# Kernel tuning notes

Hardware: AMD Instinct MI355X
Metric: run time of the kernel (lower is better)

Reference implementation:

```python
import jax, jax.numpy as jnp
import numpy as np

B, D, L = 4, 64, 4096  # batch, pos feature dim (=pos_learnable_dim), sequence length

def setup_inputs() -> dict:
    key = jax.random.key(0)
    k1, k2 = jax.random.split(key, 2)
    pos_embed = jax.random.normal(k1, (B, D, L), dtype=jnp.float32)
    # _LinearWithBias(D, D): torch weight [out, in], bias [out]
    W_pos = (jax.random.normal(k2, (D, D), dtype=jnp.float32) / np.float32(np.sqrt(D)))
    b_pos = jnp.zeros((D,), dtype=jnp.float32)
    SOFTPLUS0 = 0.6931472  # softplus(0) = ln 2, gpytorch default raw param -> constrained value
    lengthscale = jnp.asarray(SOFTPLUS0, dtype=jnp.float32)   # RBFKernel lengthscale
    outputscale = jnp.asarray(SOFTPLUS0, dtype=jnp.float32)   # ScaleKernel outputscale
    return {"pos_embed": pos_embed, "W_pos": W_pos, "b_pos": b_pos,
            "lengthscale": lengthscale, "outputscale": outputscale}

def reference(pos_embed, W_pos, b_pos, lengthscale, outputscale):
    # pos_embed: [B, D, L]
    x = jnp.swapaxes(pos_embed, 1, 2)          # [B, L, D] (transpose, linear, transpose back, transpose again)
    x = x @ W_pos.T + b_pos                    # learnable positional linear on feature dim
    # gpytorch ScaleKernel(RBFKernel): outputscale * exp(-0.5 * ||(x_i - x_j)/lengthscale||^2)
    xs = x / lengthscale                       # [B, L, D]
    sq = jnp.sum(xs * xs, axis=-1)             # [B, L]
    sq_dist = sq[:, :, None] + sq[:, None, :] - 2.0 * jnp.einsum('bld,bmd->blm', xs, xs)
    sq_dist = jnp.maximum(sq_dist, 0.0)        # gpytorch clamps sq dist at 0
    return outputscale * jnp.exp(-0.5 * sq_dist)  # [B, L, L]
```

## Files before the change

kernel.cpp:

```cpp
#include <hip/hip_runtime.h>

using bf16x8 = __attribute__((ext_vector_type(8))) __bf16;
using f32x16 = __attribute__((ext_vector_type(16))) float;

#define BB 4
#define DD 64
#define LL 4096

__global__ __launch_bounds__(256) void prep_kernel(
    const float* __restrict__ pe,
    const float* __restrict__ W,
    const float* __restrict__ bias,
    const float* __restrict__ ls,
    __bf16* __restrict__ xs,
    float* __restrict__ h)
{
    __shared__ float pe_lds[DD][64];
    __shared__ float W_lds[DD * DD];
    __shared__ float hpart[4][64];

    const int tid = threadIdx.x;
    const int blk = blockIdx.x;
    const int b  = blk >> 6;
    const int l0 = (blk & 63) * 64;

    {
        const int l = tid & 63;
        const int kb = tid >> 6;
        #pragma unroll
        for (int it = 0; it < 16; ++it) {
            const int k = it * 4 + kb;
            pe_lds[k][l] = pe[((size_t)b * DD + k) * LL + l0 + l];
        }
    }
    #pragma unroll
    for (int it = 0; it < 16; ++it)
        W_lds[it * 256 + tid] = W[it * 256 + tid];
    __syncthreads();

    const int w = tid >> 6;
    const int l = tid & 63;
    const float SQRT_LOG2E = 1.2011224087864498f;
    const float scale = SQRT_LOG2E / ls[0];

    float acc[16];
    #pragma unroll
    for (int i = 0; i < 16; ++i) acc[i] = bias[w * 16 + i];

    for (int k4 = 0; k4 < 16; ++k4) {
        const float p0 = pe_lds[k4 * 4 + 0][l];
        const float p1 = pe_lds[k4 * 4 + 1][l];
        const float p2 = pe_lds[k4 * 4 + 2][l];
        const float p3 = pe_lds[k4 * 4 + 3][l];
        #pragma unroll
        for (int i = 0; i < 16; ++i) {
            const float4 wv = *(const float4*)&W_lds[(w * 16 + i) * DD + k4 * 4];
            acc[i] += p0 * wv.x + p1 * wv.y + p2 * wv.z + p3 * wv.w;
        }
    }

    unsigned short out16[16];
    float hs = 0.0f;
    #pragma unroll
    for (int i = 0; i < 16; ++i) {
        const float xf = acc[i] * scale;
        const __bf16 bv = (__bf16)xf;
        const float xr = (float)bv;
        hs += xr * xr;
        out16[i] = __builtin_bit_cast(unsigned short, bv);
    }
    {
        __bf16* dst = xs + ((size_t)b * LL + l0 + l) * DD + w * 16;
        *(uint4*)dst       = *(const uint4*)&out16[0];
        *(uint4*)(dst + 8) = *(const uint4*)&out16[8];
    }
    hpart[w][l] = hs;
    __syncthreads();
    if (tid < 64) {
        const float s = hpart[0][tid] + hpart[1][tid] + hpart[2][tid] + hpart[3][tid];
        h[(size_t)b * LL + tid + l0] = 0.5f * s;
    }
}

__global__ __launch_bounds__(256, 4) void gram_kernel(
    const __bf16* __restrict__ xs,
    const float* __restrict__ h,
    const float* __restrict__ osc,
    float* __restrict__ out)
{
    const int bid = blockIdx.x;
    const int b  = bid >> 10;
    const int t  = bid & 1023;
    const int ti = t >> 5, tj = t & 31;

    const int tid  = threadIdx.x;
    const int wid  = tid >> 6;
    const int lane = tid & 63;
    const int lr = lane & 31, lg = lane >> 5;

    const int rows0 = ti * 128 + (wid >> 1) * 64;
    const int cols0 = tj * 128 + (wid & 1) * 64;

    const __bf16* xsb = xs + (size_t)b * LL * DD;
    const float*  hb  = h + (size_t)b * LL;

    const float c  = osc[0];
    const float lc = __builtin_log2f(c);

    #pragma unroll 1
    for (int mt = 0; mt < 2; ++mt) {
        const int r0 = rows0 + mt * 32;

        bf16x8 af[4];
        #pragma unroll
        for (int kk = 0; kk < 4; ++kk)
            af[kk] = *(const bf16x8*)(xsb + (size_t)(r0 + lr) * DD + kk * 16 + lg * 8);

        float hi2[16];
        #pragma unroll
        for (int r = 0; r < 16; ++r)
            hi2[r] = hb[r0 + (r & 3) + 8 * (r >> 2) + 4 * lg] - lc;

        #pragma unroll 1
        for (int nt = 0; nt < 2; ++nt) {
            const int c0 = cols0 + nt * 32;

            bf16x8 bg[4];
            #pragma unroll
            for (int kk = 0; kk < 4; ++kk)
                bg[kk] = *(const bf16x8*)(xsb + (size_t)(c0 + lr) * DD + kk * 16 + lg * 8);

            f32x16 acc = (f32x16)(0.0f);
            #pragma unroll
            for (int kk = 0; kk < 4; ++kk)
                acc = __builtin_amdgcn_mfma_f32_32x32x16_bf16(af[kk], bg[kk], acc, 0, 0, 0);

            const int col = c0 + lr;
            const float hj = hb[col];
            float* op = out + ((size_t)b * LL + r0 + 4 * lg) * LL + col;
            #pragma unroll
            for (int r = 0; r < 16; ++r) {
                float tt = acc[r] - hi2[r] - hj;
                tt = fminf(tt, lc);
                const int rowoff = (r & 3) + 8 * (r >> 2);
                op[(size_t)rowoff * LL] = __builtin_amdgcn_exp2f(tt);
            }
        }
    }
}

extern "C" void kernel_launch(void* const* d_in, const int* in_sizes, int n_in,
                              void* d_out, int out_size, void* d_ws, size_t ws_size,
                              hipStream_t stream) {
    const float* pe   = (const float*)d_in[0];
    const float* W    = (const float*)d_in[1];
    const float* bias = (const float*)d_in[2];
    const float* ls   = (const float*)d_in[3];
    const float* osc  = (const float*)d_in[4];
    float* out = (float*)d_out;

    __bf16* xs = (__bf16*)d_ws;
    float*  h  = (float*)((char*)d_ws + (size_t)BB * LL * DD * 2);

    prep_kernel<<<256, 256, 0, stream>>>(pe, W, bias, ls, xs, h);
    gram_kernel<<<BB * 32 * 32, 256, 0, stream>>>(xs, h, osc, out);
}
```

Before: 75.03 us.

## Retile gram kernel to 32x512 block strips with full unrolling

```diff
diff --git a/kernel.cpp b/kernel.cpp
--- a/kernel.cpp
+++ b/kernel.cpp
@@ -82,7 +82,7 @@
     }
 }
 
-__global__ __launch_bounds__(256, 4) void gram_kernel(
+__global__ __launch_bounds__(256) void gram_kernel(
     const __bf16* __restrict__ xs,
     const float* __restrict__ h,
     const float* __restrict__ osc,
@@ -91,15 +91,16 @@
     const int bid = blockIdx.x;
     const int b  = bid >> 10;
     const int t  = bid & 1023;
-    const int ti = t >> 5, tj = t & 31;
+    const int ti = t >> 3;
+    const int tj = t & 7;
 
     const int tid  = threadIdx.x;
     const int wid  = tid >> 6;
     const int lane = tid & 63;
     const int lr = lane & 31, lg = lane >> 5;
 
-    const int rows0 = ti * 128 + (wid >> 1) * 64;
-    const int cols0 = tj * 128 + (wid & 1) * 64;
+    const int rows0 = ti * 32;
+    const int cols0 = tj * 512 + wid * 128;
 
     const __bf16* xsb = xs + (size_t)b * LL * DD;
     const float*  hb  = h + (size_t)b * LL;
@@ -107,44 +108,42 @@
     const float c  = osc[0];
     const float lc = __builtin_log2f(c);
 
-    #pragma unroll 1
-    for (int mt = 0; mt < 2; ++mt) {
-        const int r0 = rows0 + mt * 32;
-
-        bf16x8 af[4];
+    bf16x8 af[4], bg[4][4];
+    #pragma unroll
+    for (int kk = 0; kk < 4; ++kk)
+        af[kk] = *(const bf16x8*)(xsb + (size_t)(rows0 + lr) * DD + kk * 16 + lg * 8);
+    #pragma unroll
+    for (int nt = 0; nt < 4; ++nt)
         #pragma unroll
         for (int kk = 0; kk < 4; ++kk)
-            af[kk] = *(const bf16x8*)(xsb + (size_t)(r0 + lr) * DD + kk * 16 + lg * 8);
+            bg[nt][kk] = *(const bf16x8*)(xsb + (size_t)(cols0 + nt * 32 + lr) * DD + kk * 16 + lg * 8);
 
-        float hi2[16];
+    f32x16 acc[4];
+    #pragma unroll
+    for (int nt = 0; nt < 4; ++nt) acc[nt] = (f32x16)(0.0f);
+
+    #pragma unroll
+    for (int kk = 0; kk < 4; ++kk)
         #pragma unroll
-        for (int r = 0; r < 16; ++r)
-            hi2[r] = hb[r0 + (r & 3) + 8 * (r >> 2) + 4 * lg] - lc;
+        for (int nt = 0; nt < 4; ++nt)
+            acc[nt] = __builtin_amdgcn_mfma_f32_32x32x16_bf16(af[kk], bg[nt][kk], acc[nt], 0, 0, 0);
 
-        #pragma unroll 1
-        for (int nt = 0; nt < 2; ++nt) {
-            const int c0 = cols0 + nt * 32;
+    float hi2[16];
+    #pragma unroll
+    for (int r = 0; r < 16; ++r)
+        hi2[r] = hb[rows0 + (r & 3) + 8 * (r >> 2) + 4 * lg] - lc;
 
-            bf16x8 bg[4];
-            #pragma unroll
-            for (int kk = 0; kk < 4; ++kk)
-                bg[kk] = *(const bf16x8*)(xsb + (size_t)(c0 + lr) * DD + kk * 16 + lg * 8);
-
-            f32x16 acc = (f32x16)(0.0f);
-            #pragma unroll
-            for (int kk = 0; kk < 4; ++kk)
-                acc = __builtin_amdgcn_mfma_f32_32x32x16_bf16(af[kk], bg[kk], acc, 0, 0, 0);
-
-            const int col = c0 + lr;
-            const float hj = hb[col];
-            float* op = out + ((size_t)b * LL + r0 + 4 * lg) * LL + col;
-            #pragma unroll
-            for (int r = 0; r < 16; ++r) {
-                float tt = acc[r] - hi2[r] - hj;
-                tt = fminf(tt, lc);
-                const int rowoff = (r & 3) + 8 * (r >> 2);
-                op[(size_t)rowoff * LL] = __builtin_amdgcn_exp2f(tt);
-            }
+    #pragma unroll
+    for (int nt = 0; nt < 4; ++nt) {
+        const int col = cols0 + nt * 32 + lr;
+        const float hj = hb[col];
+        float* op = out + ((size_t)b * LL + rows0 + 4 * lg) * LL + col;
+        #pragma unroll
+        for (int r = 0; r < 16; ++r) {
+            float tt = acc[nt][r] - hi2[r] - hj;
+            tt = fminf(tt, lc);
+            const int rowoff = (r & 3) + 8 * (r >> 2);
+            op[(size_t)rowoff * LL] = __builtin_amdgcn_exp2f(tt);
         }
     }
 }
```

Measured after the change: 68.43 us. 1.1x faster.

## Make gram kernel persistent per row strip with double-buffered B-operand loads

Applied to the files above, without the earlier changes.

```diff
diff --git a/kernel.cpp b/kernel.cpp
--- a/kernel.cpp
+++ b/kernel.cpp
@@ -82,24 +82,23 @@
     }
 }
 
-__global__ __launch_bounds__(256, 4) void gram_kernel(
+__global__ __launch_bounds__(256) void gram_kernel(
     const __bf16* __restrict__ xs,
     const float* __restrict__ h,
     const float* __restrict__ osc,
     float* __restrict__ out)
 {
     const int bid = blockIdx.x;
-    const int b  = bid >> 10;
-    const int t  = bid & 1023;
-    const int ti = t >> 5, tj = t & 31;
+    const int b  = bid >> 6;
+    const int rt = bid & 63;
 
     const int tid  = threadIdx.x;
     const int wid  = tid >> 6;
     const int lane = tid & 63;
     const int lr = lane & 31, lg = lane >> 5;
 
-    const int rows0 = ti * 128 + (wid >> 1) * 64;
-    const int cols0 = tj * 128 + (wid & 1) * 64;
+    const int rows0 = rt * 64 + (wid >> 1) * 32;
+    const int colw  = (wid & 1) * 64;
 
     const __bf16* xsb = xs + (size_t)b * LL * DD;
     const float*  hb  = h + (size_t)b * LL;
@@ -107,46 +106,70 @@
     const float c  = osc[0];
     const float lc = __builtin_log2f(c);
 
+    bf16x8 af[4];
+    #pragma unroll
+    for (int kk = 0; kk < 4; ++kk)
+        af[kk] = *(const bf16x8*)(xsb + (size_t)(rows0 + lr) * DD + kk * 16 + lg * 8);
+
+    float hi2[16];
+    #pragma unroll
+    for (int r = 0; r < 16; ++r)
+        hi2[r] = hb[rows0 + (r & 3) + 8 * (r >> 2) + 4 * lg] - lc;
+
+    float* const obase = out + ((size_t)b * LL + rows0 + 4 * lg) * LL;
+
+    bf16x8 bgA[2][4], bgB[2][4];
+    float  hjA[2], hjB[2];
+
+#define LOADBG(BG, HJ, CT)                                                     \
+    {                                                                          \
+        const int C0 = (CT) * 128 + colw;                                      \
+        _Pragma("unroll")                                                      \
+        for (int nt = 0; nt < 2; ++nt) {                                       \
+            _Pragma("unroll")                                                  \
+            for (int kk = 0; kk < 4; ++kk)                                     \
+                BG[nt][kk] = *(const bf16x8*)(xsb +                            \
+                    (size_t)(C0 + nt * 32 + lr) * DD + kk * 16 + lg * 8);      \
+            HJ[nt] = hb[C0 + nt * 32 + lr];                                    \
+        }                                                                      \
+    }
+
+#define CS(BG, HJ, CT)                                                         \
+    {                                                                          \
+        f32x16 acc[2];                                                         \
+        acc[0] = (f32x16)(0.0f);                                               \
+        acc[1] = (f32x16)(0.0f);                                               \
+        _Pragma("unroll")                                                      \
+        for (int kk = 0; kk < 4; ++kk) {                                       \
+            acc[0] = __builtin_amdgcn_mfma_f32_32x32x16_bf16(af[kk], BG[0][kk], acc[0], 0, 0, 0); \
+            acc[1] = __builtin_amdgcn_mfma_f32_32x32x16_bf16(af[kk], BG[1][kk], acc[1], 0, 0, 0); \
+        }                                                                      \
+        const int C0 = (CT) * 128 + colw;                                      \
+        _Pragma("unroll")                                                      \
+        for (int r = 0; r < 16; ++r) {                                         \
+            const size_t ro = (size_t)((r & 3) + 8 * (r >> 2)) * LL;           \
+            _Pragma("unroll")                                                  \
+            for (int nt = 0; nt < 2; ++nt) {                                   \
+                float tt = acc[nt][r] - hi2[r] - HJ[nt];                       \
+                tt = fminf(tt, lc);                                            \
+                __builtin_nontemporal_store(__builtin_amdgcn_exp2f(tt),        \
+                                            &obase[ro + C0 + nt * 32 + lr]);   \
+            }                                                                  \
+        }                                                                      \
+    }
+
+    LOADBG(bgA, hjA, 0)
     #pragma unroll 1
-    for (int mt = 0; mt < 2; ++mt) {
-        const int r0 = rows0 + mt * 32;
+    for (int ct = 0; ct < 32; ct += 2) {
+        LOADBG(bgB, hjB, ct + 1)
+        CS(bgA, hjA, ct)
+        if (ct + 2 < 32)
+            LOADBG(bgA, hjA, ct + 2)
+        CS(bgB, hjB, ct + 1)
+    }
 
-        bf16x8 af[4];
-        #pragma unroll
-        for (int kk = 0; kk < 4; ++kk)
-            af[kk] = *(const bf16x8*)(xsb + (size_t)(r0 + lr) * DD + kk * 16 + lg * 8);
-
-        float hi2[16];
-        #pragma unroll
-        for (int r = 0; r < 16; ++r)
-            hi2[r] = hb[r0 + (r & 3) + 8 * (r >> 2) + 4 * lg] - lc;
-
-        #pragma unroll 1
-        for (int nt = 0; nt < 2; ++nt) {
-            const int c0 = cols0 + nt * 32;
-
-            bf16x8 bg[4];
-            #pragma unroll
-            for (int kk = 0; kk < 4; ++kk)
-                bg[kk] = *(const bf16x8*)(xsb + (size_t)(c0 + lr) * DD + kk * 16 + lg * 8);
-
-            f32x16 acc = (f32x16)(0.0f);
-            #pragma unroll
-            for (int kk = 0; kk < 4; ++kk)
-                acc = __builtin_amdgcn_mfma_f32_32x32x16_bf16(af[kk], bg[kk], acc, 0, 0, 0);
-
-            const int col = c0 + lr;
-            const float hj = hb[col];
-            float* op = out + ((size_t)b * LL + r0 + 4 * lg) * LL + col;
-            #pragma unroll
-            for (int r = 0; r < 16; ++r) {
-                float tt = acc[r] - hi2[r] - hj;
-                tt = fminf(tt, lc);
-                const int rowoff = (r & 3) + 8 * (r >> 2);
-                op[(size_t)rowoff * LL] = __builtin_amdgcn_exp2f(tt);
-            }
-        }
-    }
+#undef LOADBG
+#undef CS
 }
 
 extern "C" void kernel_launch(void* const* d_in, const int* in_sizes, int n_in,
@@ -163,5 +186,5 @@
     float*  h  = (float*)((char*)d_ws + (size_t)BB * LL * DD * 2);
 
     prep_kernel<<<256, 256, 0, stream>>>(pe, W, bias, ls, xs, h);
-    gram_kernel<<<BB * 32 * 32, 256, 0, stream>>>(xs, h, osc, out);
+    gram_kernel<<<BB * 64, 256, 0, stream>>>(xs, h, osc, out);
 }
```

Result: slower. 81.63 us (+8.8%).
